# Kernel optimization log

Measured on AMD Instinct MI355X. Metric: run time of the kernel, lower is better.

Reference implementation:

```python
import jax, jax.numpy as jnp
import numpy as np

G = 16          # groups
K = 5           # kernel_size
IPG = 1024 // G # in_channels_per_group
OPG = 1024 // G # out_channels_per_group


def setup_inputs() -> dict:
    key = jax.random.key(0)
    k1, k2, k3 = jax.random.split(key, 3)
    inputs = jax.random.normal(k1, (4, 4096, 1024), dtype=jnp.float32)
    positions = jnp.sort(
        jax.random.randint(k2, (4, 4096), 0, 8192, dtype=jnp.int32), axis=-1)
    # kaiming-uniform-like init for kernel [G, OPG, IPG, K]
    fan_in = IPG * K
    bound = float(np.sqrt(6.0 / fan_in))
    kernel = jax.random.uniform(k3, (G, OPG, IPG, K), dtype=jnp.float32,
                                minval=-bound, maxval=bound)
    return {"inputs": inputs, "positions": positions, "kernel": kernel}


def reference(inputs, positions, kernel):
    B, L, C = inputs.shape
    c = K // 2
    # pad sequence dim; pad positions with -1 sentinel (never matches expected)
    pi = jnp.pad(inputs, ((0, 0), (c, c), (0, 0)))            # [B, L+2c, C]
    pp = jnp.pad(positions, ((0, 0), (c, c)), constant_values=-1)  # [B, L+2c]
    # sliding-window gather indices (equivalent to unfold with stride 1)
    idx = jnp.arange(L)[:, None] + jnp.arange(K)[None, :]      # [L, K]
    ip = pi[:, idx, :]        # [B, L, K, C] input patches
    ppatch = pp[:, idx]       # [B, L, K]  position patches
    # center of each patch is the original position at that output index
    offsets = jnp.arange(-c, c + 1, dtype=positions.dtype)    # [K]
    expected = positions[:, :, None] + offsets                # [B, L, K]
    mask = (ppatch == expected).astype(inputs.dtype)          # [B, L, K]
    masked = ip * mask[..., None]                             # [B, L, K, C]
    # split channels into groups: [B, L, K, G, IPG]
    gp = masked.reshape(B, L, K, G, IPG)
    # grouped conv reduce over in_channels_per_group and kernel taps
    out = jnp.einsum('blkgi,goik->blgo', gp, kernel)           # [B, L, G, OPG]
    return out
```

## Files before the change

### kernel.cpp

```cpp
#include <hip/hip_runtime.h>

typedef __attribute__((ext_vector_type(8))) short short8;
typedef __attribute__((ext_vector_type(4))) float float4v;
typedef __attribute__((ext_vector_type(4))) unsigned short us4;

namespace {
constexpr int NG   = 16;
constexpr int LSEQ = 4096;
constexpr int CIN  = 1024;
constexpr int IPG  = 64;
constexpr int OPG  = 64;
constexpr int KT   = 5;
constexpr int ROWS = 128;
constexpr int SIN_STRIDE = 72;
constexpr int SIN_ROWS   = ROWS + KT - 1;
constexpr int KSTEPS = 10;
constexpr size_t WFRAG_SHORTS = (size_t)NG * 4 * KSTEPS * 512;
constexpr size_t WFRAG_BYTES  = WFRAG_SHORTS * 2;
}

__device__ __forceinline__ unsigned short f2bf(float f) {
  unsigned int u = __builtin_bit_cast(unsigned int, f);
  u += 0x7fffu + ((u >> 16) & 1u);
  return (unsigned short)(u >> 16);
}

__global__ __launch_bounds__(256) void wprep(const float* __restrict__ gwt,
                                             unsigned short* __restrict__ wfrag) {
  const int u = blockIdx.x * 256 + threadIdx.x;
  const int E    = u * 8;
  const int tile = E >> 9;
  const int w9   = E & 511;
  const int n    = w9 >> 5;
  const int quad = (w9 & 31) >> 3;
  const int ks   = tile % KSTEPS;
  const int tt   = tile / KSTEPS;
  const int t    = tt & 3;
  const int g    = tt >> 2;
  const int tap  = ks >> 1;
  const int h    = ks & 1;
  const int o    = t * 16 + n;
  const float* src = gwt + (((size_t)(g * 64 + o) * 64) + h * 32 + quad * 8) * KT + tap;
  short8 v;
  #pragma unroll
  for (int j = 0; j < 8; ++j)
    v[j] = (short)f2bf(src[j * KT]);
  *(short8*)(wfrag + E) = v;
}

__global__ __launch_bounds__(256, 4) void mconv_main(
    const float* __restrict__ gin,
    const int* __restrict__ gpos,
    const unsigned short* __restrict__ wfrag,
    float* __restrict__ gout) {
  __shared__ __align__(16) unsigned short sIn[SIN_ROWS * SIN_STRIDE];
  __shared__ unsigned char sMaskB[ROWS];

  const int tid  = threadIdx.x;
  const int wv   = tid >> 6;
  const int lane = tid & 63;
  const int quad = lane >> 4;
  const int l16  = lane & 15;
  const int wm   = wv & 1;
  const int wn   = wv >> 1;

  const int g  = blockIdx.y;
  const int b  = blockIdx.z;
  const int l0 = blockIdx.x * ROWS;
  const int bL = b * LSEQ;

  for (int u = tid; u < SIN_ROWS * 16; u += 256) {
    const int r  = u >> 4;
    const int c4 = u & 15;
    const int l  = l0 - 2 + r;
    us4 w = {0, 0, 0, 0};
    if (l >= 0 && l < LSEQ) {
      float4v v = *(const float4v*)(gin + (size_t)(bL + l) * CIN + g * IPG + c4 * 4);
      w[0] = f2bf(v[0]); w[1] = f2bf(v[1]); w[2] = f2bf(v[2]); w[3] = f2bf(v[3]);
    }
    const int p = (c4 * 4 + ((r & 3) << 4)) & 63;
    *(us4*)(&sIn[r * SIN_STRIDE + p]) = w;
  }

  if (tid < ROWS) {
    const int l = l0 + tid;
    const int pc = gpos[bL + l];
    unsigned int mbits = 0;
    #pragma unroll
    for (int tap = 0; tap < KT; ++tap) {
      const int lsrc = l + tap - 2;
      int ok = 0;
      if (lsrc >= 0 && lsrc < LSEQ)
        ok = (gpos[bL + lsrc] == pc + (tap - 2));
      mbits |= (unsigned int)ok << tap;
    }
    sMaskB[tid] = (unsigned char)mbits;
  }
  __syncthreads();

  int mb[4];
  #pragma unroll
  for (int mt = 0; mt < 4; ++mt)
    mb[mt] = sMaskB[wm * 64 + mt * 16 + l16];

  const int laneoff = l16 * 32 + quad * 8;
  const unsigned short* wb0 = wfrag + (size_t)((g * 4 + wn * 2) * KSTEPS) * 512 + laneoff;
  const unsigned short* wb1 = wb0 + (size_t)KSTEPS * 512;

  const short8 zero8 = {0, 0, 0, 0, 0, 0, 0, 0};
  const float4v zf = {0.f, 0.f, 0.f, 0.f};
  float4v acc[4][2];
  #pragma unroll
  for (int mt = 0; mt < 4; ++mt) { acc[mt][0] = zf; acc[mt][1] = zf; }

  short8 bc0 = *(const short8*)(wb0);
  short8 bc1 = *(const short8*)(wb1);

  #pragma unroll 2
  for (int ks = 0; ks < KSTEPS; ++ks) {
    const int ksn = (ks + 1 < KSTEPS) ? ks + 1 : KSTEPS - 1;
    short8 bn0 = *(const short8*)(wb0 + ksn * 512);
    short8 bn1 = *(const short8*)(wb1 + ksn * 512);
    const int tap = ks >> 1;
    const int h   = ks & 1;
    const int s   = h * 32 + quad * 8;
    #pragma unroll
    for (int mt = 0; mt < 4; ++mt) {
      const int r  = wm * 64 + mt * 16 + l16 + tap;
      const int sp = (s + ((r & 3) << 4)) & 63;
      short8 a = *(const short8*)(&sIn[r * SIN_STRIDE + sp]);
      if (!((mb[mt] >> tap) & 1)) a = zero8;
      acc[mt][0] = __builtin_amdgcn_mfma_f32_16x16x32_bf16(a, bc0, acc[mt][0], 0, 0, 0);
      acc[mt][1] = __builtin_amdgcn_mfma_f32_16x16x32_bf16(a, bc1, acc[mt][1], 0, 0, 0);
    }
    bc0 = bn0; bc1 = bn1;
  }

  #pragma unroll
  for (int mt = 0; mt < 4; ++mt) {
    const int lrow = l0 + wm * 64 + mt * 16 + quad * 4;
    #pragma unroll
    for (int reg = 0; reg < 4; ++reg) {
      float* orow = gout + (size_t)(bL + lrow + reg) * CIN + g * OPG + wn * 32;
      orow[l16]      = acc[mt][0][reg];
      orow[16 + l16] = acc[mt][1][reg];
    }
  }
}

namespace fb {
constexpr int ROWS_PER_CHUNK = 128;
constexpr int CHUNKS = 4;
constexpr int ROWS_PER_BLOCK = 512;
constexpr int SW_STRIDE  = 328;
constexpr int FSIN_STRIDE = 72;
constexpr int FSIN_ROWS   = 132;
}

__global__ __launch_bounds__(256, 2) void mconv_f32_mfma(
    const float* __restrict__ gin, const int* __restrict__ gpos,
    const float* __restrict__ gwt, float* __restrict__ gout) {
  using namespace fb;
  __shared__ __align__(16) unsigned short sW[OPG * SW_STRIDE];
  __shared__ __align__(16) unsigned short sIn[FSIN_ROWS * FSIN_STRIDE];
  __shared__ unsigned char sMask[ROWS_PER_CHUNK * KT];

  const int tid  = threadIdx.x;
  const int wave = tid >> 6;
  const int lane = tid & 63;
  const int quad = lane >> 4;
  const int l16  = lane & 15;
  const int g  = blockIdx.y;
  const int b  = blockIdx.z;
  const int tile0 = blockIdx.x * ROWS_PER_BLOCK;
  const int bL = b * LSEQ;

  {
    const float* wg = gwt + (size_t)g * (OPG * IPG * KT);
    for (int u = tid; u < (OPG * IPG * KT) / 4; u += 256) {
      const int base = u * 4;
      float4v v = *(const float4v*)(wg + base);
      int o = base / (IPG * KT);
      int r = base - o * (IPG * KT);
      int i = r / KT;
      int k = r - i * KT;
      int addr = o * SW_STRIDE + k * IPG + i;
      #pragma unroll
      for (int t = 0; t < 4; ++t) {
        sW[addr] = f2bf(v[t]);
        ++k; addr += IPG;
        if (k == KT) { k = 0; ++i; addr -= KT * IPG - 1; }
      }
    }
  }
  const short8 zero8 = {0,0,0,0,0,0,0,0};
  const float4v zf = {0.f,0.f,0.f,0.f};
  for (int ch = 0; ch < CHUNKS; ++ch) {
    const int l0 = tile0 + ch * ROWS_PER_CHUNK;
    __syncthreads();
    for (int t = tid; t < ROWS_PER_CHUNK * KT; t += 256) {
      const int lr = t / KT, tap = t - lr * KT, l = l0 + lr, lsrc = l + tap - 2;
      int ok = 0;
      if (lsrc >= 0 && lsrc < LSEQ) ok = (gpos[bL + lsrc] == gpos[bL + l] + (tap - 2));
      sMask[t] = (unsigned char)ok;
    }
    for (int u = tid; u < FSIN_ROWS * 16; u += 256) {
      const int r = u >> 4, c4 = u & 15, l = l0 - 2 + r;
      us4 w = {0,0,0,0};
      if (l >= 0 && l < LSEQ) {
        float4v v = *(const float4v*)(gin + (size_t)(bL + l) * CIN + g * IPG + c4 * 4);
        w[0]=f2bf(v[0]); w[1]=f2bf(v[1]); w[2]=f2bf(v[2]); w[3]=f2bf(v[3]);
      }
      *(us4*)(&sIn[r * FSIN_STRIDE + c4 * 4]) = w;
    }
    __syncthreads();
    float4v acc[2][4];
    #pragma unroll
    for (int mm = 0; mm < 2; ++mm)
      #pragma unroll
      for (int nt = 0; nt < 4; ++nt) acc[mm][nt] = zf;
    const int m0 = wave * 32 + l16, m1 = m0 + 16;
    #pragma unroll
    for (int tap = 0; tap < KT; ++tap) {
      const bool msk0 = sMask[m0 * KT + tap] != 0;
      const bool msk1 = sMask[m1 * KT + tap] != 0;
      #pragma unroll
      for (int h = 0; h < 2; ++h) {
        const int kk = tap * IPG + h * 32 + quad * 8;
        const short8 b0 = *(const short8*)(&sW[(0*16 + l16) * SW_STRIDE + kk]);
        const short8 b1 = *(const short8*)(&sW[(1*16 + l16) * SW_STRIDE + kk]);
        const short8 b2 = *(const short8*)(&sW[(2*16 + l16) * SW_STRIDE + kk]);
        const short8 b3 = *(const short8*)(&sW[(3*16 + l16) * SW_STRIDE + kk]);
        const int ci = h * 32 + quad * 8;
        short8 a0 = *(const short8*)(&sIn[(m0 + tap) * FSIN_STRIDE + ci]);
        short8 a1 = *(const short8*)(&sIn[(m1 + tap) * FSIN_STRIDE + ci]);
        if (!msk0) a0 = zero8;
        if (!msk1) a1 = zero8;
        acc[0][0] = __builtin_amdgcn_mfma_f32_16x16x32_bf16(a0,b0,acc[0][0],0,0,0);
        acc[0][1] = __builtin_amdgcn_mfma_f32_16x16x32_bf16(a0,b1,acc[0][1],0,0,0);
        acc[0][2] = __builtin_amdgcn_mfma_f32_16x16x32_bf16(a0,b2,acc[0][2],0,0,0);
        acc[0][3] = __builtin_amdgcn_mfma_f32_16x16x32_bf16(a0,b3,acc[0][3],0,0,0);
        acc[1][0] = __builtin_amdgcn_mfma_f32_16x16x32_bf16(a1,b0,acc[1][0],0,0,0);
        acc[1][1] = __builtin_amdgcn_mfma_f32_16x16x32_bf16(a1,b1,acc[1][1],0,0,0);
        acc[1][2] = __builtin_amdgcn_mfma_f32_16x16x32_bf16(a1,b2,acc[1][2],0,0,0);
        acc[1][3] = __builtin_amdgcn_mfma_f32_16x16x32_bf16(a1,b3,acc[1][3],0,0,0);
      }
    }
    #pragma unroll
    for (int mm = 0; mm < 2; ++mm) {
      const int lrow = l0 + wave * 32 + mm * 16 + quad * 4;
      #pragma unroll
      for (int reg = 0; reg < 4; ++reg) {
        float* orow = gout + ((size_t)(bL + lrow + reg) * NG + g) * OPG;
        #pragma unroll
        for (int nt = 0; nt < 4; ++nt)
          orow[nt * 16 + l16] = acc[mm][nt][reg];
      }
    }
  }
}

extern "C" void kernel_launch(void* const* d_in, const int* in_sizes, int n_in,
                              void* d_out, int out_size, void* d_ws, size_t ws_size,
                              hipStream_t stream) {
  (void)in_sizes; (void)n_in; (void)out_size;
  const float* gin  = (const float*)d_in[0];
  const int*   gpos = (const int*)d_in[1];
  const float* gwt  = (const float*)d_in[2];
  float*       gout = (float*)d_out;

  if (ws_size >= WFRAG_BYTES) {
    unsigned short* wfrag = (unsigned short*)d_ws;
    hipLaunchKernelGGL(wprep, dim3(160), dim3(256), 0, stream, gwt, wfrag);
    dim3 grid(LSEQ / ROWS, NG, 4);
    hipLaunchKernelGGL(mconv_main, grid, dim3(256), 0, stream,
                       gin, gpos, wfrag, gout);
  } else {
    dim3 grid(LSEQ / fb::ROWS_PER_BLOCK, NG, 4);
    hipLaunchKernelGGL(mconv_f32_mfma, grid, dim3(256), 0, stream,
                       gin, gpos, gwt, gout);
  }
}
```

Baseline: 132.6 us.

## Precompute tap masks and double-buffer two row chunks per block

```diff
diff --git a/kernel.cpp b/kernel.cpp
--- a/kernel.cpp
+++ b/kernel.cpp
@@ -12,11 +12,13 @@
 constexpr int OPG  = 64;
 constexpr int KT   = 5;
 constexpr int ROWS = 128;
+constexpr int CH   = 2;
 constexpr int SIN_STRIDE = 72;
 constexpr int SIN_ROWS   = ROWS + KT - 1;
 constexpr int KSTEPS = 10;
 constexpr size_t WFRAG_SHORTS = (size_t)NG * 4 * KSTEPS * 512;
 constexpr size_t WFRAG_BYTES  = WFRAG_SHORTS * 2;
+constexpr size_t MASK_BYTES   = (size_t)4 * LSEQ;
 }
 
 __device__ __forceinline__ unsigned short f2bf(float f) {
@@ -46,6 +48,144 @@
   for (int j = 0; j < 8; ++j)
     v[j] = (short)f2bf(src[j * KT]);
   *(short8*)(wfrag + E) = v;
+}
+
+__global__ __launch_bounds__(256) void mprep(const int* __restrict__ gpos,
+                                             unsigned char* __restrict__ gmask) {
+  const int id = blockIdx.x * 256 + threadIdx.x;
+  const int b  = id >> 12;
+  const int l  = id & (LSEQ - 1);
+  const int base = b * LSEQ;
+  const int pc = gpos[base + l];
+  unsigned int mbits = 0;
+  #pragma unroll
+  for (int tap = 0; tap < KT; ++tap) {
+    const int lsrc = l + tap - 2;
+    int ok = 0;
+    if (lsrc >= 0 && lsrc < LSEQ)
+      ok = (gpos[base + lsrc] == pc + (tap - 2));
+    mbits |= (unsigned int)ok << tap;
+  }
+  gmask[id] = (unsigned char)mbits;
+}
+
+__global__ __launch_bounds__(256, 4) void mconv_main2(
+    const float* __restrict__ gin,
+    const unsigned char* __restrict__ gmask,
+    const unsigned short* __restrict__ wfrag,
+    float* __restrict__ gout) {
+  __shared__ __align__(16) unsigned short sIn[2][SIN_ROWS * SIN_STRIDE];
+
+  const int tid  = threadIdx.x;
+  const int wv   = tid >> 6;
+  const int lane = tid & 63;
+  const int quad = lane >> 4;
+  const int l16  = lane & 15;
+  const int wm   = wv & 1;
+  const int wn   = wv >> 1;
+
+  const int g  = blockIdx.y;
+  const int b  = blockIdx.z;
+  const int l0 = blockIdx.x * (ROWS * CH);
+  const int bL = b * LSEQ;
+
+  const float* ginb = gin + (size_t)bL * CIN + g * IPG;
+
+  float4v st[9];
+  auto issue = [&](int l0c) {
+    #pragma unroll
+    for (int k = 0; k < 9; ++k) {
+      const int u = tid + k * 256;
+      if (u < SIN_ROWS * 16) {
+        const int r  = u >> 4;
+        const int c4 = u & 15;
+        const int l  = l0c - 2 + r;
+        float4v v = {0.f, 0.f, 0.f, 0.f};
+        if (l >= 0 && l < LSEQ)
+          v = *(const float4v*)(ginb + (size_t)l * CIN + c4 * 4);
+        st[k] = v;
+      }
+    }
+  };
+  auto stage_write = [&](int bsel) {
+    #pragma unroll
+    for (int k = 0; k < 9; ++k) {
+      const int u = tid + k * 256;
+      if (u < SIN_ROWS * 16) {
+        const int r  = u >> 4;
+        const int c4 = u & 15;
+        const int p  = (c4 * 4 + ((r & 3) << 4)) & 63;
+        us4 w;
+        w[0] = f2bf(st[k][0]); w[1] = f2bf(st[k][1]);
+        w[2] = f2bf(st[k][2]); w[3] = f2bf(st[k][3]);
+        *(us4*)(&sIn[bsel][r * SIN_STRIDE + p]) = w;
+      }
+    }
+  };
+
+  int mb0[4], mb1[4];
+  #pragma unroll
+  for (int mt = 0; mt < 4; ++mt) {
+    const int rr = wm * 64 + mt * 16 + l16;
+    mb0[mt] = gmask[bL + l0 + rr];
+    mb1[mt] = gmask[bL + l0 + ROWS + rr];
+  }
+
+  const int laneoff = l16 * 32 + quad * 8;
+  const unsigned short* wb0 = wfrag + (size_t)((g * 4 + wn * 2) * KSTEPS) * 512 + laneoff;
+  const unsigned short* wb1 = wb0 + (size_t)KSTEPS * 512;
+  const short8 zero8 = {0, 0, 0, 0, 0, 0, 0, 0};
+  const float4v zf = {0.f, 0.f, 0.f, 0.f};
+
+  auto compute_store = [&](int bsel, int l0c, const int* mb) {
+    float4v acc[4][2];
+    #pragma unroll
+    for (int mt = 0; mt < 4; ++mt) { acc[mt][0] = zf; acc[mt][1] = zf; }
+    short8 bc0 = *(const short8*)(wb0);
+    short8 bc1 = *(const short8*)(wb1);
+    #pragma unroll 2
+    for (int ks = 0; ks < KSTEPS; ++ks) {
+      const int ksn = (ks + 1 < KSTEPS) ? ks + 1 : KSTEPS - 1;
+      short8 bn0 = *(const short8*)(wb0 + ksn * 512);
+      short8 bn1 = *(const short8*)(wb1 + ksn * 512);
+      const int tap = ks >> 1;
+      const int h   = ks & 1;
+      const int s   = h * 32 + quad * 8;
+      #pragma unroll
+      for (int mt = 0; mt < 4; ++mt) {
+        const int r  = wm * 64 + mt * 16 + l16 + tap;
+        const int sp = (s + ((r & 3) << 4)) & 63;
+        short8 a = *(const short8*)(&sIn[bsel][r * SIN_STRIDE + sp]);
+        if (!((mb[mt] >> tap) & 1)) a = zero8;
+        acc[mt][0] = __builtin_amdgcn_mfma_f32_16x16x32_bf16(a, bc0, acc[mt][0], 0, 0, 0);
+        acc[mt][1] = __builtin_amdgcn_mfma_f32_16x16x32_bf16(a, bc1, acc[mt][1], 0, 0, 0);
+      }
+      bc0 = bn0; bc1 = bn1;
+    }
+    #pragma unroll
+    for (int mt = 0; mt < 4; ++mt) {
+      const int lrow = l0c + wm * 64 + mt * 16 + quad * 4;
+      #pragma unroll
+      for (int reg = 0; reg < 4; ++reg) {
+        float* orow = gout + (size_t)(bL + lrow + reg) * CIN + g * OPG + wn * 32;
+        orow[l16]      = acc[mt][0][reg];
+        orow[16 + l16] = acc[mt][1][reg];
+      }
+    }
+  };
+
+  issue(l0);
+  stage_write(0);
+  asm volatile("s_waitcnt lgkmcnt(0)" ::: "memory");
+  __builtin_amdgcn_s_barrier();
+
+  issue(l0 + ROWS);
+  compute_store(0, l0, mb0);
+  stage_write(1);
+  asm volatile("s_waitcnt lgkmcnt(0)" ::: "memory");
+  __builtin_amdgcn_s_barrier();
+
+  compute_store(1, l0 + ROWS, mb1);
 }
 
 __global__ __launch_bounds__(256, 4) void mconv_main(
@@ -269,7 +409,15 @@
   const float* gwt  = (const float*)d_in[2];
   float*       gout = (float*)d_out;
 
-  if (ws_size >= WFRAG_BYTES) {
+  if (ws_size >= WFRAG_BYTES + MASK_BYTES) {
+    unsigned short* wfrag = (unsigned short*)d_ws;
+    unsigned char*  gmask = (unsigned char*)d_ws + WFRAG_BYTES;
+    hipLaunchKernelGGL(wprep, dim3(160), dim3(256), 0, stream, gwt, wfrag);
+    hipLaunchKernelGGL(mprep, dim3(64), dim3(256), 0, stream, gpos, gmask);
+    dim3 grid(LSEQ / (ROWS * CH), NG, 4);
+    hipLaunchKernelGGL(mconv_main2, grid, dim3(256), 0, stream,
+                       gin, gmask, wfrag, gout);
+  } else if (ws_size >= WFRAG_BYTES) {
     unsigned short* wfrag = (unsigned short*)d_ws;
     hipLaunchKernelGGL(wprep, dim3(160), dim3(256), 0, stream, gwt, wfrag);
     dim3 grid(LSEQ / ROWS, NG, 4);
```

New measurement: 123.1 us. 7.2% less time.

## Precompute masks in prep kernel and double-buffer input chunks per block

Applied to the files above, without the earlier changes.

```diff
diff --git a/kernel.cpp b/kernel.cpp
--- a/kernel.cpp
+++ b/kernel.cpp
@@ -12,11 +12,13 @@
 constexpr int OPG  = 64;
 constexpr int KT   = 5;
 constexpr int ROWS = 128;
+constexpr int CH   = 4;
 constexpr int SIN_STRIDE = 72;
 constexpr int SIN_ROWS   = ROWS + KT - 1;
 constexpr int KSTEPS = 10;
 constexpr size_t WFRAG_SHORTS = (size_t)NG * 4 * KSTEPS * 512;
 constexpr size_t WFRAG_BYTES  = WFRAG_SHORTS * 2;
+constexpr size_t MASK_BYTES   = (size_t)4 * LSEQ;
 }
 
 __device__ __forceinline__ unsigned short f2bf(float f) {
@@ -25,36 +27,55 @@
   return (unsigned short)(u >> 16);
 }
 
-__global__ __launch_bounds__(256) void wprep(const float* __restrict__ gwt,
-                                             unsigned short* __restrict__ wfrag) {
-  const int u = blockIdx.x * 256 + threadIdx.x;
-  const int E    = u * 8;
-  const int tile = E >> 9;
-  const int w9   = E & 511;
-  const int n    = w9 >> 5;
-  const int quad = (w9 & 31) >> 3;
-  const int ks   = tile % KSTEPS;
-  const int tt   = tile / KSTEPS;
-  const int t    = tt & 3;
-  const int g    = tt >> 2;
-  const int tap  = ks >> 1;
-  const int h    = ks & 1;
-  const int o    = t * 16 + n;
-  const float* src = gwt + (((size_t)(g * 64 + o) * 64) + h * 32 + quad * 8) * KT + tap;
-  short8 v;
-  #pragma unroll
-  for (int j = 0; j < 8; ++j)
-    v[j] = (short)f2bf(src[j * KT]);
-  *(short8*)(wfrag + E) = v;
-}
-
-__global__ __launch_bounds__(256, 4) void mconv_main(
+__global__ __launch_bounds__(256) void prep_fused(const float* __restrict__ gwt,
+                                                  const int* __restrict__ gpos,
+                                                  unsigned short* __restrict__ wfrag,
+                                                  unsigned char* __restrict__ gmask) {
+  if (blockIdx.x < 160) {
+    const int u = blockIdx.x * 256 + threadIdx.x;
+    const int E    = u * 8;
+    const int tile = E >> 9;
+    const int w9   = E & 511;
+    const int n    = w9 >> 5;
+    const int quad = (w9 & 31) >> 3;
+    const int ks   = tile % KSTEPS;
+    const int tt   = tile / KSTEPS;
+    const int t    = tt & 3;
+    const int g    = tt >> 2;
+    const int tap  = ks >> 1;
+    const int h    = ks & 1;
+    const int o    = t * 16 + n;
+    const float* src = gwt + (((size_t)(g * 64 + o) * 64) + h * 32 + quad * 8) * KT + tap;
+    short8 v;
+    #pragma unroll
+    for (int j = 0; j < 8; ++j)
+      v[j] = (short)f2bf(src[j * KT]);
+    *(short8*)(wfrag + E) = v;
+  } else {
+    const int id = (blockIdx.x - 160) * 256 + threadIdx.x;
+    const int b  = id >> 12;
+    const int l  = id & (LSEQ - 1);
+    const int base = b * LSEQ;
+    const int pc = gpos[base + l];
+    unsigned int mbits = 0;
+    #pragma unroll
+    for (int tap = 0; tap < KT; ++tap) {
+      const int lsrc = l + tap - 2;
+      int ok = 0;
+      if (lsrc >= 0 && lsrc < LSEQ)
+        ok = (gpos[base + lsrc] == pc + (tap - 2));
+      mbits |= (unsigned int)ok << tap;
+    }
+    gmask[id] = (unsigned char)mbits;
+  }
+}
+
+__global__ __launch_bounds__(256, 4) void mconv_main4(
     const float* __restrict__ gin,
-    const int* __restrict__ gpos,
+    const unsigned char* __restrict__ gmask,
     const unsigned short* __restrict__ wfrag,
     float* __restrict__ gout) {
-  __shared__ __align__(16) unsigned short sIn[SIN_ROWS * SIN_STRIDE];
-  __shared__ unsigned char sMaskB[ROWS];
+  __shared__ __align__(16) unsigned short sIn[2][SIN_ROWS * SIN_STRIDE];
 
   const int tid  = threadIdx.x;
   const int wv   = tid >> 6;
@@ -66,84 +87,110 @@
 
   const int g  = blockIdx.y;
   const int b  = blockIdx.z;
-  const int l0 = blockIdx.x * ROWS;
+  const int l0 = blockIdx.x * (ROWS * CH);
   const int bL = b * LSEQ;
 
-  for (int u = tid; u < SIN_ROWS * 16; u += 256) {
-    const int r  = u >> 4;
-    const int c4 = u & 15;
-    const int l  = l0 - 2 + r;
-    us4 w = {0, 0, 0, 0};
-    if (l >= 0 && l < LSEQ) {
-      float4v v = *(const float4v*)(gin + (size_t)(bL + l) * CIN + g * IPG + c4 * 4);
-      w[0] = f2bf(v[0]); w[1] = f2bf(v[1]); w[2] = f2bf(v[2]); w[3] = f2bf(v[3]);
-    }
-    const int p = (c4 * 4 + ((r & 3) << 4)) & 63;
-    *(us4*)(&sIn[r * SIN_STRIDE + p]) = w;
-  }
-
-  if (tid < ROWS) {
-    const int l = l0 + tid;
-    const int pc = gpos[bL + l];
-    unsigned int mbits = 0;
-    #pragma unroll
-    for (int tap = 0; tap < KT; ++tap) {
-      const int lsrc = l + tap - 2;
-      int ok = 0;
-      if (lsrc >= 0 && lsrc < LSEQ)
-        ok = (gpos[bL + lsrc] == pc + (tap - 2));
-      mbits |= (unsigned int)ok << tap;
-    }
-    sMaskB[tid] = (unsigned char)mbits;
-  }
-  __syncthreads();
-
-  int mb[4];
-  #pragma unroll
-  for (int mt = 0; mt < 4; ++mt)
-    mb[mt] = sMaskB[wm * 64 + mt * 16 + l16];
+  const float* ginb = gin + (size_t)bL * CIN + g * IPG;
+
+  float4v st[9];
+  auto issue = [&](int l0c) {
+    #pragma unroll
+    for (int k = 0; k < 9; ++k) {
+      const int u = tid + k * 256;
+      if (u < SIN_ROWS * 16) {
+        const int r  = u >> 4;
+        const int c4 = u & 15;
+        const int l  = l0c - 2 + r;
+        float4v v = {0.f, 0.f, 0.f, 0.f};
+        if (l >= 0 && l < LSEQ)
+          v = *(const float4v*)(ginb + (size_t)l * CIN + c4 * 4);
+        st[k] = v;
+      }
+    }
+  };
+  auto stage_write = [&](int bsel) {
+    #pragma unroll
+    for (int k = 0; k < 9; ++k) {
+      const int u = tid + k * 256;
+      if (u < SIN_ROWS * 16) {
+        const int r  = u >> 4;
+        const int c4 = u & 15;
+        const int p  = (c4 * 4 + ((r & 3) << 4)) & 63;
+        us4 w;
+        w[0] = f2bf(st[k][0]); w[1] = f2bf(st[k][1]);
+        w[2] = f2bf(st[k][2]); w[3] = f2bf(st[k][3]);
+        *(us4*)(&sIn[bsel][r * SIN_STRIDE + p]) = w;
+      }
+    }
+  };
 
   const int laneoff = l16 * 32 + quad * 8;
   const unsigned short* wb0 = wfrag + (size_t)((g * 4 + wn * 2) * KSTEPS) * 512 + laneoff;
   const unsigned short* wb1 = wb0 + (size_t)KSTEPS * 512;
-
   const short8 zero8 = {0, 0, 0, 0, 0, 0, 0, 0};
   const float4v zf = {0.f, 0.f, 0.f, 0.f};
-  float4v acc[4][2];
+
+  auto compute_store = [&](int bsel, int l0c, int mbpc) {
+    float4v acc[4][2];
+    #pragma unroll
+    for (int mt = 0; mt < 4; ++mt) { acc[mt][0] = zf; acc[mt][1] = zf; }
+    short8 bc0 = *(const short8*)(wb0);
+    short8 bc1 = *(const short8*)(wb1);
+    #pragma unroll 2
+    for (int ks = 0; ks < KSTEPS; ++ks) {
+      const int ksn = (ks + 1 < KSTEPS) ? ks + 1 : KSTEPS - 1;
+      short8 bn0 = *(const short8*)(wb0 + ksn * 512);
+      short8 bn1 = *(const short8*)(wb1 + ksn * 512);
+      const int tap = ks >> 1;
+      const int h   = ks & 1;
+      const int s   = h * 32 + quad * 8;
+      #pragma unroll
+      for (int mt = 0; mt < 4; ++mt) {
+        const int r  = wm * 64 + mt * 16 + l16 + tap;
+        const int sp = (s + ((r & 3) << 4)) & 63;
+        short8 a = *(const short8*)(&sIn[bsel][r * SIN_STRIDE + sp]);
+        if (!((mbpc >> (mt * 8 + tap)) & 1)) a = zero8;
+        acc[mt][0] = __builtin_amdgcn_mfma_f32_16x16x32_bf16(a, bc0, acc[mt][0], 0, 0, 0);
+        acc[mt][1] = __builtin_amdgcn_mfma_f32_16x16x32_bf16(a, bc1, acc[mt][1], 0, 0, 0);
+      }
+      bc0 = bn0; bc1 = bn1;
+    }
+    #pragma unroll
+    for (int mt = 0; mt < 4; ++mt) {
+      const int lrow = l0c + wm * 64 + mt * 16 + quad * 4;
+      #pragma unroll
+      for (int reg = 0; reg < 4; ++reg) {
+        float* orow = gout + (size_t)(bL + lrow + reg) * CIN + g * OPG + wn * 32;
+        orow[l16]      = acc[mt][0][reg];
+        orow[16 + l16] = acc[mt][1][reg];
+      }
+    }
+  };
+
+  issue(l0);
+
+  int mbp[CH];
   #pragma unroll
-  for (int mt = 0; mt < 4; ++mt) { acc[mt][0] = zf; acc[mt][1] = zf; }
-
-  short8 bc0 = *(const short8*)(wb0);
-  short8 bc1 = *(const short8*)(wb1);
-
-  #pragma unroll 2
-  for (int ks = 0; ks < KSTEPS; ++ks) {
-    const int ksn = (ks + 1 < KSTEPS) ? ks + 1 : KSTEPS - 1;
-    short8 bn0 = *(const short8*)(wb0 + ksn * 512);
-    short8 bn1 = *(const short8*)(wb1 + ksn * 512);
-    const int tap = ks >> 1;
-    const int h   = ks & 1;
-    const int s   = h * 32 + quad * 8;
-    #pragma unroll
-    for (int mt = 0; mt < 4; ++mt) {
-      const int r  = wm * 64 + mt * 16 + l16 + tap;
-      const int sp = (s + ((r & 3) << 4)) & 63;
-      short8 a = *(const short8*)(&sIn[r * SIN_STRIDE + sp]);
-      if (!((mb[mt] >> tap) & 1)) a = zero8;
-      acc[mt][0] = __builtin_amdgcn_mfma_f32_16x16x32_bf16(a, bc0, acc[mt][0], 0, 0, 0);
-      acc[mt][1] = __builtin_amdgcn_mfma_f32_16x16x32_bf16(a, bc1, acc[mt][1], 0, 0, 0);
-    }
-    bc0 = bn0; bc1 = bn1;
-  }
+  for (int c = 0; c < CH; ++c) {
+    int m = 0;
+    #pragma unroll
+    for (int mt = 0; mt < 4; ++mt)
+      m |= (int)gmask[bL + l0 + c * ROWS + wm * 64 + mt * 16 + l16] << (mt * 8);
+    mbp[c] = m;
+  }
+
+  stage_write(0);
+  asm volatile("s_waitcnt lgkmcnt(0)" ::: "memory");
+  __builtin_amdgcn_s_barrier();
 
   #pragma unroll
-  for (int mt = 0; mt < 4; ++mt) {
-    const int lrow = l0 + wm * 64 + mt * 16 + quad * 4;
-    #pragma unroll
-    for (int reg = 0; reg < 4; ++reg) {
-      float* orow = gout + (size_t)(bL + lrow + reg) * CIN + g * OPG + wn * 32;
-      orow[l16]      = acc[mt][0][reg];
-      orow[16 + l16] = acc[mt][1][reg];
+  for (int c = 0; c < CH; ++c) {
+    if (c + 1 < CH) issue(l0 + (c + 1) * ROWS);
+    compute_store(c & 1, l0 + c * ROWS, mbp[c]);
+    if (c + 1 < CH) {
+      stage_write((c + 1) & 1);
+      asm volatile("s_waitcnt lgkmcnt(0)" ::: "memory");
+      __builtin_amdgcn_s_barrier();
     }
   }
 }
@@ -269,12 +316,14 @@
   const float* gwt  = (const float*)d_in[2];
   float*       gout = (float*)d_out;
 
-  if (ws_size >= WFRAG_BYTES) {
+  if (ws_size >= WFRAG_BYTES + MASK_BYTES) {
     unsigned short* wfrag = (unsigned short*)d_ws;
-    hipLaunchKernelGGL(wprep, dim3(160), dim3(256), 0, stream, gwt, wfrag);
-    dim3 grid(LSEQ / ROWS, NG, 4);
-    hipLaunchKernelGGL(mconv_main, grid, dim3(256), 0, stream,
-                       gin, gpos, wfrag, gout);
+    unsigned char*  gmask = (unsigned char*)d_ws + WFRAG_BYTES;
+    hipLaunchKernelGGL(prep_fused, dim3(224), dim3(256), 0, stream,
+                       gwt, gpos, wfrag, gmask);
+    dim3 grid(LSEQ / (ROWS * CH), NG, 4);
+    hipLaunchKernelGGL(mconv_main4, grid, dim3(256), 0, stream,
+                       gin, gmask, wfrag, gout);
   } else {
     dim3 grid(LSEQ / fb::ROWS_PER_BLOCK, NG, 4);
     hipLaunchKernelGGL(mconv_f32_mfma, grid, dim3(256), 0, stream,
```

Measured after the change: 133.9 us. About the same (+1.0%).

## Stage fp32 input via direct global-to-LDS loads and precompute mask in prep kernel

Applied to the files above, without the earlier changes.

```diff
diff --git a/kernel.cpp b/kernel.cpp
--- a/kernel.cpp
+++ b/kernel.cpp
@@ -3,6 +3,7 @@
 typedef __attribute__((ext_vector_type(8))) short short8;
 typedef __attribute__((ext_vector_type(4))) float float4v;
 typedef __attribute__((ext_vector_type(4))) unsigned short us4;
+typedef __attribute__((ext_vector_type(4))) unsigned int uint4v;
 
 namespace {
 constexpr int NG   = 16;
@@ -12,11 +13,11 @@
 constexpr int OPG  = 64;
 constexpr int KT   = 5;
 constexpr int ROWS = 128;
-constexpr int SIN_STRIDE = 72;
-constexpr int SIN_ROWS   = ROWS + KT - 1;
+constexpr int SIN_SLOTS  = 132 * 16;
 constexpr int KSTEPS = 10;
 constexpr size_t WFRAG_SHORTS = (size_t)NG * 4 * KSTEPS * 512;
 constexpr size_t WFRAG_BYTES  = WFRAG_SHORTS * 2;
+constexpr size_t MASK_BYTES   = (size_t)4 * LSEQ;
 }
 
 __device__ __forceinline__ unsigned short f2bf(float f) {
@@ -25,36 +26,55 @@
   return (unsigned short)(u >> 16);
 }
 
-__global__ __launch_bounds__(256) void wprep(const float* __restrict__ gwt,
-                                             unsigned short* __restrict__ wfrag) {
-  const int u = blockIdx.x * 256 + threadIdx.x;
-  const int E    = u * 8;
-  const int tile = E >> 9;
-  const int w9   = E & 511;
-  const int n    = w9 >> 5;
-  const int quad = (w9 & 31) >> 3;
-  const int ks   = tile % KSTEPS;
-  const int tt   = tile / KSTEPS;
-  const int t    = tt & 3;
-  const int g    = tt >> 2;
-  const int tap  = ks >> 1;
-  const int h    = ks & 1;
-  const int o    = t * 16 + n;
-  const float* src = gwt + (((size_t)(g * 64 + o) * 64) + h * 32 + quad * 8) * KT + tap;
-  short8 v;
-  #pragma unroll
-  for (int j = 0; j < 8; ++j)
-    v[j] = (short)f2bf(src[j * KT]);
-  *(short8*)(wfrag + E) = v;
-}
-
-__global__ __launch_bounds__(256, 4) void mconv_main(
+__global__ __launch_bounds__(256) void prep_fused(const float* __restrict__ gwt,
+                                                  const int* __restrict__ gpos,
+                                                  unsigned short* __restrict__ wfrag,
+                                                  unsigned char* __restrict__ gmask) {
+  if (blockIdx.x < 160) {
+    const int u = blockIdx.x * 256 + threadIdx.x;
+    const int E    = u * 8;
+    const int tile = E >> 9;
+    const int w9   = E & 511;
+    const int n    = w9 >> 5;
+    const int quad = (w9 & 31) >> 3;
+    const int ks   = tile % KSTEPS;
+    const int tt   = tile / KSTEPS;
+    const int t    = tt & 3;
+    const int g    = tt >> 2;
+    const int tap  = ks >> 1;
+    const int h    = ks & 1;
+    const int o    = t * 16 + n;
+    const float* src = gwt + (((size_t)(g * 64 + o) * 64) + h * 32 + quad * 8) * KT + tap;
+    short8 v;
+    #pragma unroll
+    for (int j = 0; j < 8; ++j)
+      v[j] = (short)f2bf(src[j * KT]);
+    *(short8*)(wfrag + E) = v;
+  } else {
+    const int id = (blockIdx.x - 160) * 256 + threadIdx.x;
+    const int b  = id >> 12;
+    const int l  = id & (LSEQ - 1);
+    const int base = b * LSEQ;
+    const int pc = gpos[base + l];
+    unsigned int mbits = 0;
+    #pragma unroll
+    for (int tap = 0; tap < KT; ++tap) {
+      const int lsrc = l + tap - 2;
+      int ok = 0;
+      if (lsrc >= 0 && lsrc < LSEQ)
+        ok = (gpos[base + lsrc] == pc + (tap - 2));
+      mbits |= (unsigned int)ok << tap;
+    }
+    gmask[id] = (unsigned char)mbits;
+  }
+}
+
+__global__ __launch_bounds__(256) void mconv_main6(
     const float* __restrict__ gin,
-    const int* __restrict__ gpos,
+    const unsigned char* __restrict__ gmask,
     const unsigned short* __restrict__ wfrag,
     float* __restrict__ gout) {
-  __shared__ __align__(16) unsigned short sIn[SIN_ROWS * SIN_STRIDE];
-  __shared__ unsigned char sMaskB[ROWS];
+  __shared__ __align__(16) float sIn[SIN_SLOTS * 4];
 
   const int tid  = threadIdx.x;
   const int wv   = tid >> 6;
@@ -69,50 +89,43 @@
   const int l0 = blockIdx.x * ROWS;
   const int bL = b * LSEQ;
 
-  for (int u = tid; u < SIN_ROWS * 16; u += 256) {
+  const float* ginb = gin + (size_t)bL * CIN + g * IPG;
+
+  auto stage_one = [&](int u) {
     const int r  = u >> 4;
-    const int c4 = u & 15;
-    const int l  = l0 - 2 + r;
-    us4 w = {0, 0, 0, 0};
-    if (l >= 0 && l < LSEQ) {
-      float4v v = *(const float4v*)(gin + (size_t)(bL + l) * CIN + g * IPG + c4 * 4);
-      w[0] = f2bf(v[0]); w[1] = f2bf(v[1]); w[2] = f2bf(v[2]); w[3] = f2bf(v[3]);
-    }
-    const int p = (c4 * 4 + ((r & 3) << 4)) & 63;
-    *(us4*)(&sIn[r * SIN_STRIDE + p]) = w;
-  }
-
-  if (tid < ROWS) {
-    const int l = l0 + tid;
-    const int pc = gpos[bL + l];
-    unsigned int mbits = 0;
-    #pragma unroll
-    for (int tap = 0; tap < KT; ++tap) {
-      const int lsrc = l + tap - 2;
-      int ok = 0;
-      if (lsrc >= 0 && lsrc < LSEQ)
-        ok = (gpos[bL + lsrc] == pc + (tap - 2));
-      mbits |= (unsigned int)ok << tap;
-    }
-    sMaskB[tid] = (unsigned char)mbits;
-  }
-  __syncthreads();
+    const int ps = u & 15;
+    const int c4 = ps ^ (r & 7);
+    int l = l0 - 2 + r;
+    l = l < 0 ? 0 : (l > LSEQ - 1 ? LSEQ - 1 : l);
+    const float* src = ginb + (size_t)l * CIN + c4 * 4;
+    __builtin_amdgcn_global_load_lds(
+        (const __attribute__((address_space(1))) void*)(const void*)src,
+        (__attribute__((address_space(3))) void*)(void*)&sIn[u * 4],
+        16, 0, 0);
+  };
+
+  #pragma unroll
+  for (int k = 0; k < 8; ++k)
+    stage_one(tid + k * 256);
+  if (wv == 0)
+    stage_one(tid + 2048);
 
   int mb[4];
   #pragma unroll
   for (int mt = 0; mt < 4; ++mt)
-    mb[mt] = sMaskB[wm * 64 + mt * 16 + l16];
+    mb[mt] = gmask[bL + l0 + wm * 64 + mt * 16 + l16];
 
   const int laneoff = l16 * 32 + quad * 8;
   const unsigned short* wb0 = wfrag + (size_t)((g * 4 + wn * 2) * KSTEPS) * 512 + laneoff;
   const unsigned short* wb1 = wb0 + (size_t)KSTEPS * 512;
-
   const short8 zero8 = {0, 0, 0, 0, 0, 0, 0, 0};
   const float4v zf = {0.f, 0.f, 0.f, 0.f};
+
+  __syncthreads();
+
   float4v acc[4][2];
   #pragma unroll
   for (int mt = 0; mt < 4; ++mt) { acc[mt][0] = zf; acc[mt][1] = zf; }
-
   short8 bc0 = *(const short8*)(wb0);
   short8 bc1 = *(const short8*)(wb1);
 
@@ -123,12 +136,21 @@
     short8 bn1 = *(const short8*)(wb1 + ksn * 512);
     const int tap = ks >> 1;
     const int h   = ks & 1;
-    const int s   = h * 32 + quad * 8;
+    const int ls  = h * 8 + quad * 2;
     #pragma unroll
     for (int mt = 0; mt < 4; ++mt) {
-      const int r  = wm * 64 + mt * 16 + l16 + tap;
-      const int sp = (s + ((r & 3) << 4)) & 63;
-      short8 a = *(const short8*)(&sIn[r * SIN_STRIDE + sp]);
+      const int r   = wm * 64 + mt * 16 + l16 + tap;
+      const int swz = r & 7;
+      const float* rowp = &sIn[r * 64];
+      float4v lo = *(const float4v*)(rowp + ((ls ^ swz) << 2));
+      float4v hi = *(const float4v*)(rowp + (((ls + 1) ^ swz) << 2));
+      unsigned int d0, d1, d2, d3;
+      asm("v_cvt_pk_bf16_f32 %0, %1, %2" : "=v"(d0) : "v"(lo[0]), "v"(lo[1]));
+      asm("v_cvt_pk_bf16_f32 %0, %1, %2" : "=v"(d1) : "v"(lo[2]), "v"(lo[3]));
+      asm("v_cvt_pk_bf16_f32 %0, %1, %2" : "=v"(d2) : "v"(hi[0]), "v"(hi[1]));
+      asm("v_cvt_pk_bf16_f32 %0, %1, %2" : "=v"(d3) : "v"(hi[2]), "v"(hi[3]));
+      uint4v dv = {d0, d1, d2, d3};
+      short8 a = __builtin_bit_cast(short8, dv);
       if (!((mb[mt] >> tap) & 1)) a = zero8;
       acc[mt][0] = __builtin_amdgcn_mfma_f32_16x16x32_bf16(a, bc0, acc[mt][0], 0, 0, 0);
       acc[mt][1] = __builtin_amdgcn_mfma_f32_16x16x32_bf16(a, bc1, acc[mt][1], 0, 0, 0);
@@ -269,12 +291,14 @@
   const float* gwt  = (const float*)d_in[2];
   float*       gout = (float*)d_out;
 
-  if (ws_size >= WFRAG_BYTES) {
+  if (ws_size >= WFRAG_BYTES + MASK_BYTES) {
     unsigned short* wfrag = (unsigned short*)d_ws;
-    hipLaunchKernelGGL(wprep, dim3(160), dim3(256), 0, stream, gwt, wfrag);
+    unsigned char*  gmask = (unsigned char*)d_ws + WFRAG_BYTES;
+    hipLaunchKernelGGL(prep_fused, dim3(224), dim3(256), 0, stream,
+                       gwt, gpos, wfrag, gmask);
     dim3 grid(LSEQ / ROWS, NG, 4);
-    hipLaunchKernelGGL(mconv_main, grid, dim3(256), 0, stream,
-                       gin, gpos, wfrag, gout);
+    hipLaunchKernelGGL(mconv_main6, grid, dim3(256), 0, stream,
+                       gin, gmask, wfrag, gout);
   } else {
     dim3 grid(LSEQ / fb::ROWS_PER_BLOCK, NG, 4);
     hipLaunchKernelGGL(mconv_f32_mfma, grid, dim3(256), 0, stream,
```

Measured after the change: 128.0 us. -3.5%, faster.
